# Kernel optimization log

Measured on AMD Instinct MI355X. Metric: run time of the kernel, lower is better.

Reference implementation:

```python
import jax, jax.numpy as jnp
import numpy as np

T, N, E, F_IN, C = 8, 50000, 800000, 64, 64


def setup_inputs() -> dict:
    key = jax.random.key(0)
    ks = jax.random.split(key, 32)
    inp = {
        "x": jax.random.normal(ks[0], (T, N, F_IN), dtype=jnp.float32),
        "edge_index": jax.random.randint(ks[1], (2, E), 0, N, dtype=jnp.int32),
        "edge_weight": jax.random.uniform(ks[2], (E,), dtype=jnp.float32),
    }
    s = 0.05
    names = ["xz", "hz", "xr", "hr", "xh", "hh"]
    for i, nm in enumerate(names):
        cin = F_IN if nm[0] == "x" else C
        inp[f"W{nm}0"] = jax.random.normal(ks[3 + 3 * i], (cin, C), dtype=jnp.float32) * s
        inp[f"W{nm}1"] = jax.random.normal(ks[4 + 3 * i], (cin, C), dtype=jnp.float32) * s
        inp[f"b{nm}"] = jax.random.normal(ks[5 + 3 * i], (C,), dtype=jnp.float32) * s
    inp["W_lin"] = jax.random.normal(ks[30], (C, 1), dtype=jnp.float32) * s
    inp["b_lin"] = jax.random.normal(ks[31], (1,), dtype=jnp.float32) * s
    return inp


def reference(x, edge_index, edge_weight,
              Wxz0, Wxz1, bxz, Whz0, Whz1, bhz,
              Wxr0, Wxr1, bxr, Whr0, Whr1, bhr,
              Wxh0, Wxh1, bxh, Whh0, Whh1, bhh,
              W_lin, b_lin):
    src, dst = edge_index[0], edge_index[1]
    n = x.shape[1]
    # sym-normalized L_hat = -D^{-1/2} A D^{-1/2} (ChebConv, lambda_max=2)
    deg = jnp.zeros((n,), x.dtype).at[src].add(edge_weight)
    dinv = jnp.where(deg > 0, jax.lax.rsqrt(jnp.maximum(deg, 1e-12)), 0.0)
    nw = -edge_weight * dinv[src] * dinv[dst]  # (E,)

    def cheb(v, W0, W1, b):
        # K=2 Chebyshev: v @ W0 + (L_hat v) @ W1 + b ; v: (T, N, Cin)
        msgs = nw[None, :, None] * v[:, src, :]          # (T, E, Cin)
        tx1 = jnp.zeros_like(v).at[:, dst, :].add(msgs)  # scatter-add over nodes
        return v @ W0 + tx1 @ W1 + b

    H = jnp.zeros(x.shape[:2] + (Whz0.shape[0],), x.dtype)  # H=None -> zeros
    Z = jax.nn.sigmoid(cheb(x, Wxz0, Wxz1, bxz) + cheb(H, Whz0, Whz1, bhz))
    R = jax.nn.sigmoid(cheb(x, Wxr0, Wxr1, bxr) + cheb(H, Whr0, Whr1, bhr))
    Ht = jnp.tanh(cheb(x, Wxh0, Wxh1, bxh) + cheb(R * H, Whh0, Whh1, bhh))
    H = Z * H + (1.0 - Z) * Ht
    h = jax.nn.relu(H)
    return h @ W_lin + b_lin
```

## Files before the change

kernel.cpp:

```cpp
#include <hip/hip_runtime.h>

#define T_ 8
#define N_ 50000
#define E_ 800000
#define C_ 64

typedef __attribute__((ext_vector_type(8))) short bf16x8;
typedef __attribute__((ext_vector_type(4))) float f32x4;

__device__ inline short f2bf(float f) {
    union { float f; unsigned int u; } v; v.f = f;
    unsigned int u = v.u + 0x7FFFu + ((v.u >> 16) & 1u);
    return (short)(u >> 16);
}
__device__ inline float bf2f_lo(unsigned int u) {
    union { unsigned int u; float f; } v; v.u = u << 16;
    return v.f;
}
__device__ inline float bf2f_hi(unsigned int u) {
    union { unsigned int u; float f; } v; v.u = u & 0xffff0000u;
    return v.f;
}

#define SCAN_TILES 49

__global__ __launch_bounds__(256) void fused_prep_kernel(
        const int* __restrict__ src, const int* __restrict__ dst,
        const float* __restrict__ w,
        float* __restrict__ degw, int* __restrict__ cnt,
        const float* __restrict__ x, unsigned short* __restrict__ xb,
        const float* __restrict__ Wz0, const float* __restrict__ Wz1,
        const float* __restrict__ Wh0, const float* __restrict__ Wh1,
        short* __restrict__ swz) {
    if (blockIdx.x < 3125) {
        int e = blockIdx.x * 256 + threadIdx.x;
        if (e < E_) {
            atomicAdd(&degw[src[e]], w[e]);
            atomicAdd(&cnt[dst[e]], 1);
        }
    } else if (blockIdx.x < 15625) {
        int id = (blockIdx.x - 3125) * 256 + threadIdx.x;
        int c8 = id & 7;
        int t = (id >> 3) & 7;
        int n = id >> 6;
        const float* xr = x + ((long long)t * N_ + n) * C_ + c8 * 8;
        float4 a = *(const float4*)(xr);
        float4 b = *(const float4*)(xr + 4);
        bf16x8 o;
        o[0] = f2bf(a.x); o[1] = f2bf(a.y); o[2] = f2bf(a.z); o[3] = f2bf(a.w);
        o[4] = f2bf(b.x); o[5] = f2bf(b.y); o[6] = f2bf(b.z); o[7] = f2bf(b.w);
        *(bf16x8*)(xb + (long long)id * 8) = o;
    } else {
        int idx = (blockIdx.x - 15625) * 256 + threadIdx.x;
        int j = idx & 7;
        int lane = (idx >> 3) & 63;
        int kb = (idx >> 9) & 1;
        int c = (idx >> 10) & 3;
        int mat = idx >> 12;
        const float* W = (mat == 0) ? Wz0 : (mat == 1) ? Wz1 : (mat == 2) ? Wh0 : Wh1;
        int k = kb * 32 + (lane >> 4) * 8 + j;
        int n = c * 16 + (lane & 15);
        swz[idx] = f2bf(W[k * 64 + n]);
    }
}

__global__ __launch_bounds__(1024) void scan_a_kernel(const int* __restrict__ cnt,
                                                      int* __restrict__ rowptr,
                                                      int* __restrict__ tsum) {
    __shared__ int wsum[16];
    int tid = threadIdx.x, lane = tid & 63, wid = tid >> 6;
    int idx = blockIdx.x * 1024 + tid;
    int orig = (idx < N_) ? cnt[idx] : 0;
    int v = orig;
#pragma unroll
    for (int off = 1; off < 64; off <<= 1) {
        int u = __shfl_up(v, off);
        if (lane >= off) v += u;
    }
    if (lane == 63) wsum[wid] = v;
    __syncthreads();
    if (wid == 0) {
        int s = (lane < 16) ? wsum[lane] : 0;
#pragma unroll
        for (int off = 1; off < 16; off <<= 1) {
            int u = __shfl_up(s, off);
            if (lane >= off) s += u;
        }
        if (lane < 16) wsum[lane] = s;
    }
    __syncthreads();
    int wpre = wid ? wsum[wid - 1] : 0;
    if (idx < N_) rowptr[idx] = wpre + v - orig;
    if (tid == 0) tsum[blockIdx.x] = wsum[15];
}

__global__ __launch_bounds__(1024) void scan_b_kernel(const int* __restrict__ tsum,
                                                      int* __restrict__ rowptr) {
    __shared__ int soff[SCAN_TILES];
    __shared__ int stot;
    int tid = threadIdx.x, lane = tid & 63, wid = tid >> 6;
    if (wid == 0) {
        int own = (lane < SCAN_TILES) ? tsum[lane] : 0;
        int s = own;
#pragma unroll
        for (int off = 1; off < 64; off <<= 1) {
            int u = __shfl_up(s, off);
            if (lane >= off) s += u;
        }
        if (lane < SCAN_TILES) soff[lane] = s - own;
        if (lane == SCAN_TILES - 1) stot = s;
    }
    __syncthreads();
    int off = soff[blockIdx.x];
    int idx = blockIdx.x * 1024 + tid;
    if (idx < N_) rowptr[idx] += off;
    if (blockIdx.x == SCAN_TILES - 1 && tid == 0) rowptr[N_] = stot;
}

__global__ void reorder_kernel(const int* __restrict__ src, const int* __restrict__ dst,
                               const float* __restrict__ w, const float* __restrict__ degw,
                               int* __restrict__ rowptr, int2* __restrict__ es, int E) {
    int e = blockIdx.x * blockDim.x + threadIdx.x;
    if (e < E) {
        int s = src[e], d = dst[e];
        float ds = degw[s], dd = degw[d];
        float is = ds > 0.f ? rsqrtf(fmaxf(ds, 1e-12f)) : 0.f;
        float id = dd > 0.f ? rsqrtf(fmaxf(dd, 1e-12f)) : 0.f;
        float nwv = -w[e] * is * id;
        int pos = atomicAdd(&rowptr[d], 1);
        es[pos] = make_int2(s, __float_as_int(nwv));
    }
}

#define ACC8(W, V)                                                       \
    acc[0] += (W) * bf2f_lo((V).x); acc[1] += (W) * bf2f_hi((V).x);      \
    acc[2] += (W) * bf2f_lo((V).y); acc[3] += (W) * bf2f_hi((V).y);      \
    acc[4] += (W) * bf2f_lo((V).z); acc[5] += (W) * bf2f_hi((V).z);      \
    acc[6] += (W) * bf2f_lo((V).w); acc[7] += (W) * bf2f_hi((V).w);

__global__ __launch_bounds__(256) void gather_node_kernel(
        const int* __restrict__ rowptr, const int2* __restrict__ es,
        const unsigned short* __restrict__ xb, const short* __restrict__ swz,
        const float* __restrict__ bxz, const float* __restrict__ bhz,
        const float* __restrict__ bxh, const float* __restrict__ bhh,
        const float* __restrict__ Wlin, const float* __restrict__ blin,
        float* __restrict__ out) {
    __shared__ unsigned short ltx[32 * 72];
    __shared__ float laz[2][16][65];

    int lane = threadIdx.x & 63;
    int wid = threadIdx.x >> 6;
    int base = blockIdx.x * 4;

    {
        int d = base + wid;
        int t = lane >> 3;
        int oct = lane & 7;
        int start = d ? rowptr[d - 1] : 0;
        int end = rowptr[d];
        float acc[8] = {0.f, 0.f, 0.f, 0.f, 0.f, 0.f, 0.f, 0.f};
        const unsigned short* xbase = xb + lane * 8;
        for (int b0 = start; b0 < end; b0 += 64) {
            int m = end - b0;
            if (m > 64) m = 64;
            int2 pk = (lane < m) ? es[b0 + lane] : make_int2(0, 0);
            int k = 0;
            for (; k + 3 < m; k += 4) {
                int s0 = __shfl(pk.x, k);
                int s1 = __shfl(pk.x, k + 1);
                int s2 = __shfl(pk.x, k + 2);
                int s3 = __shfl(pk.x, k + 3);
                uint4 v0 = *(const uint4*)(xbase + (long long)s0 * 512);
                uint4 v1 = *(const uint4*)(xbase + (long long)s1 * 512);
                uint4 v2 = *(const uint4*)(xbase + (long long)s2 * 512);
                uint4 v3 = *(const uint4*)(xbase + (long long)s3 * 512);
                float w0 = __int_as_float(__shfl(pk.y, k));
                float w1 = __int_as_float(__shfl(pk.y, k + 1));
                float w2 = __int_as_float(__shfl(pk.y, k + 2));
                float w3 = __int_as_float(__shfl(pk.y, k + 3));
                ACC8(w0, v0);
                ACC8(w1, v1);
                ACC8(w2, v2);
                ACC8(w3, v3);
            }
            for (; k < m; ++k) {
                int s0 = __shfl(pk.x, k);
                float w0 = __int_as_float(__shfl(pk.y, k));
                uint4 v0 = *(const uint4*)(xbase + (long long)s0 * 512);
                ACC8(w0, v0);
            }
        }
        uint4 o;
        o.x = (unsigned int)(unsigned short)f2bf(acc[0]) |
              ((unsigned int)(unsigned short)f2bf(acc[1]) << 16);
        o.y = (unsigned int)(unsigned short)f2bf(acc[2]) |
              ((unsigned int)(unsigned short)f2bf(acc[3]) << 16);
        o.z = (unsigned int)(unsigned short)f2bf(acc[4]) |
              ((unsigned int)(unsigned short)f2bf(acc[5]) << 16);
        o.w = (unsigned int)(unsigned short)f2bf(acc[6]) |
              ((unsigned int)(unsigned short)f2bf(acc[7]) << 16);
        int r = wid * 8 + t;
        *(uint4*)(ltx + r * 72 + oct * 8) = o;
    }
    __syncthreads();

    int mt = wid >> 1;
    int g = wid & 1;
    int c16 = lane & 15;
    int kq = lane >> 4;
    int r_blk = mt * 16 + c16;
    const unsigned short* xr = xb + (long long)(base * 8 + r_blk) * C_ + kq * 8;
    bf16x8 ax0 = *(const bf16x8*)(xr);
    bf16x8 ax1 = *(const bf16x8*)(xr + 32);
    bf16x8 at0 = *(const bf16x8*)(ltx + r_blk * 72 + kq * 8);
    bf16x8 at1 = *(const bf16x8*)(ltx + r_blk * 72 + 32 + kq * 8);

    const float* bA = g ? bxh : bxz;
    const float* bB = g ? bhh : bhz;
    const short* wA = swz + (2 * g) * 4096 + lane * 8;
    const short* wB = swz + (2 * g + 1) * 4096 + lane * 8;

    f32x4 a4[4];
#pragma unroll
    for (int c = 0; c < 4; ++c) {
        int col = c * 16 + c16;
        float bv = bA[col] + bB[col];
        a4[c] = (f32x4){bv, bv, bv, bv};
    }
#pragma unroll
    for (int c = 0; c < 4; ++c) {
        bf16x8 bA0 = *(const bf16x8*)(wA + (c * 2 + 0) * 512);
        bf16x8 bA1 = *(const bf16x8*)(wA + (c * 2 + 1) * 512);
        bf16x8 bB0 = *(const bf16x8*)(wB + (c * 2 + 0) * 512);
        bf16x8 bB1 = *(const bf16x8*)(wB + (c * 2 + 1) * 512);
        a4[c] = __builtin_amdgcn_mfma_f32_16x16x32_bf16(ax0, bA0, a4[c], 0, 0, 0);
        a4[c] = __builtin_amdgcn_mfma_f32_16x16x32_bf16(ax1, bA1, a4[c], 0, 0, 0);
        a4[c] = __builtin_amdgcn_mfma_f32_16x16x32_bf16(at0, bB0, a4[c], 0, 0, 0);
        a4[c] = __builtin_amdgcn_mfma_f32_16x16x32_bf16(at1, bB1, a4[c], 0, 0, 0);
    }

    if (g == 0) {
#pragma unroll
        for (int c = 0; c < 4; ++c)
#pragma unroll
            for (int r = 0; r < 4; ++r)
                laz[mt][kq * 4 + r][c * 16 + c16] = a4[c][r];
    }
    __syncthreads();
    if (g == 1) {
        float part[4] = {0.f, 0.f, 0.f, 0.f};
#pragma unroll
        for (int c = 0; c < 4; ++c) {
            int col = c * 16 + c16;
            float wl = Wlin[col];
#pragma unroll
            for (int r = 0; r < 4; ++r) {
                float a = laz[mt][kq * 4 + r][col];
                float b = a4[c][r];
                float z = 1.f / (1.f + __expf(-a));
                float aa = fabsf(b);
                float e = __expf(-2.f * aa);
                float ht = copysignf((1.f - e) / (1.f + e), b);
                float h = fmaxf((1.f - z) * ht, 0.f);
                part[r] += h * wl;
            }
        }
#pragma unroll
        for (int m = 1; m <= 8; m <<= 1) {
#pragma unroll
            for (int r = 0; r < 4; ++r) part[r] += __shfl_xor(part[r], m);
        }
        if (c16 == 0) {
            float bl = blin[0];
#pragma unroll
            for (int r = 0; r < 4; ++r) {
                int rb = mt * 16 + kq * 4 + r;
                out[(long long)(rb & 7) * N_ + base + (rb >> 3)] = part[r] + bl;
            }
        }
    }
}

extern "C" void kernel_launch(void* const* d_in, const int* in_sizes, int n_in,
                              void* d_out, int out_size, void* d_ws, size_t ws_size,
                              hipStream_t stream) {
    const float* x    = (const float*)d_in[0];
    const int*   ei   = (const int*)d_in[1];
    const float* w    = (const float*)d_in[2];
    const float* Wxz0 = (const float*)d_in[3];
    const float* Wxz1 = (const float*)d_in[4];
    const float* bxz  = (const float*)d_in[5];
    const float* bhz  = (const float*)d_in[8];
    const float* Wxh0 = (const float*)d_in[15];
    const float* Wxh1 = (const float*)d_in[16];
    const float* bxh  = (const float*)d_in[17];
    const float* bhh  = (const float*)d_in[20];
    const float* Wlin = (const float*)d_in[21];
    const float* blin = (const float*)d_in[22];
    float* out = (float*)d_out;

    const int* src = ei;
    const int* dst = ei + E_;

    char* ws = (char*)d_ws;
    size_t off = 0;
    auto alloc = [&](size_t bytes) {
        char* p = ws + off;
        off = (off + bytes + 511) & ~(size_t)511;
        return p;
    };
    short* swz             = (short*)alloc(4 * 4096 * sizeof(short));
    float* degw            = (float*)alloc((size_t)N_ * 4);
    int*   cnt             = (int*)alloc((size_t)N_ * 4);
    int*   rowptr          = (int*)alloc(((size_t)N_ + 1) * 4);
    int*   tsum            = (int*)alloc((size_t)SCAN_TILES * 4);
    int2*  es              = (int2*)alloc((size_t)E_ * 8);
    unsigned short* xb     = (unsigned short*)alloc((size_t)T_ * N_ * C_ * 2);

    hipMemsetAsync(degw, 0, (size_t)N_ * 4, stream);
    hipMemsetAsync(cnt, 0, (size_t)N_ * 4, stream);

    fused_prep_kernel<<<15689, 256, 0, stream>>>(src, dst, w, degw, cnt,
                                                 x, xb, Wxz0, Wxz1, Wxh0, Wxh1, swz);
    scan_a_kernel<<<SCAN_TILES, 1024, 0, stream>>>(cnt, rowptr, tsum);
    scan_b_kernel<<<SCAN_TILES, 1024, 0, stream>>>(tsum, rowptr);
    reorder_kernel<<<(E_ + 255) / 256, 256, 0, stream>>>(src, dst, w, degw, rowptr, es, E_);

    gather_node_kernel<<<N_ / 4, 256, 0, stream>>>(
        rowptr, es, xb, swz, bxz, bhz, bxh, bhh, Wlin, blin, out);
}
```

Before: 423.8 us.

## Replace CSR build with fixed-capacity per-node edge buckets and overflow list

Drops the two scan kernels and the reorder kernel by writing each edge directly into a per-destination bucket of fixed capacity during the degree-counting pass, with an overflow list for nodes beyond capacity. Edge normalization moves into the gather kernel, which computes rsqrt of source and destination degrees on the fly. The gather inner loop is unrolled to 8 outstanding loads. Risks: padded bucket storage costs memory and scattered writes, and the overflow path is a linear scan over all overflow entries for every high-degree node.

```diff
diff --git a/kernel.cpp b/kernel.cpp
--- a/kernel.cpp
+++ b/kernel.cpp
@@ -4,6 +4,7 @@
 #define N_ 50000
 #define E_ 800000
 #define C_ 64
+#define OVF_CAP 131072
 
 typedef __attribute__((ext_vector_type(8))) short bf16x8;
 typedef __attribute__((ext_vector_type(4))) float f32x4;
@@ -22,21 +23,27 @@
     return v.f;
 }
 
-#define SCAN_TILES 49
-
 __global__ __launch_bounds__(256) void fused_prep_kernel(
         const int* __restrict__ src, const int* __restrict__ dst,
         const float* __restrict__ w,
         float* __restrict__ degw, int* __restrict__ cnt,
+        int2* __restrict__ es, int cap,
+        int* __restrict__ ovfcnt, int4* __restrict__ ovf,
         const float* __restrict__ x, unsigned short* __restrict__ xb,
         const float* __restrict__ Wz0, const float* __restrict__ Wz1,
         const float* __restrict__ Wh0, const float* __restrict__ Wh1,
         short* __restrict__ swz) {
     if (blockIdx.x < 3125) {
         int e = blockIdx.x * 256 + threadIdx.x;
-        if (e < E_) {
-            atomicAdd(&degw[src[e]], w[e]);
-            atomicAdd(&cnt[dst[e]], 1);
+        int s = src[e], d = dst[e];
+        float wv = w[e];
+        atomicAdd(&degw[s], wv);
+        int pos = atomicAdd(&cnt[d], 1);
+        if (pos < cap) {
+            es[d * cap + pos] = make_int2(s, __float_as_int(wv));
+        } else {
+            int op = atomicAdd(ovfcnt, 1);
+            if (op < OVF_CAP) ovf[op] = make_int4(d, s, __float_as_int(wv), 0);
         }
     } else if (blockIdx.x < 15625) {
         int id = (blockIdx.x - 3125) * 256 + threadIdx.x;
@@ -64,74 +71,6 @@
     }
 }
 
-__global__ __launch_bounds__(1024) void scan_a_kernel(const int* __restrict__ cnt,
-                                                      int* __restrict__ rowptr,
-                                                      int* __restrict__ tsum) {
-    __shared__ int wsum[16];
-    int tid = threadIdx.x, lane = tid & 63, wid = tid >> 6;
-    int idx = blockIdx.x * 1024 + tid;
-    int orig = (idx < N_) ? cnt[idx] : 0;
-    int v = orig;
-#pragma unroll
-    for (int off = 1; off < 64; off <<= 1) {
-        int u = __shfl_up(v, off);
-        if (lane >= off) v += u;
-    }
-    if (lane == 63) wsum[wid] = v;
-    __syncthreads();
-    if (wid == 0) {
-        int s = (lane < 16) ? wsum[lane] : 0;
-#pragma unroll
-        for (int off = 1; off < 16; off <<= 1) {
-            int u = __shfl_up(s, off);
-            if (lane >= off) s += u;
-        }
-        if (lane < 16) wsum[lane] = s;
-    }
-    __syncthreads();
-    int wpre = wid ? wsum[wid - 1] : 0;
-    if (idx < N_) rowptr[idx] = wpre + v - orig;
-    if (tid == 0) tsum[blockIdx.x] = wsum[15];
-}
-
-__global__ __launch_bounds__(1024) void scan_b_kernel(const int* __restrict__ tsum,
-                                                      int* __restrict__ rowptr) {
-    __shared__ int soff[SCAN_TILES];
-    __shared__ int stot;
-    int tid = threadIdx.x, lane = tid & 63, wid = tid >> 6;
-    if (wid == 0) {
-        int own = (lane < SCAN_TILES) ? tsum[lane] : 0;
-        int s = own;
-#pragma unroll
-        for (int off = 1; off < 64; off <<= 1) {
-            int u = __shfl_up(s, off);
-            if (lane >= off) s += u;
-        }
-        if (lane < SCAN_TILES) soff[lane] = s - own;
-        if (lane == SCAN_TILES - 1) stot = s;
-    }
-    __syncthreads();
-    int off = soff[blockIdx.x];
-    int idx = blockIdx.x * 1024 + tid;
-    if (idx < N_) rowptr[idx] += off;
-    if (blockIdx.x == SCAN_TILES - 1 && tid == 0) rowptr[N_] = stot;
-}
-
-__global__ void reorder_kernel(const int* __restrict__ src, const int* __restrict__ dst,
-                               const float* __restrict__ w, const float* __restrict__ degw,
-                               int* __restrict__ rowptr, int2* __restrict__ es, int E) {
-    int e = blockIdx.x * blockDim.x + threadIdx.x;
-    if (e < E) {
-        int s = src[e], d = dst[e];
-        float ds = degw[s], dd = degw[d];
-        float is = ds > 0.f ? rsqrtf(fmaxf(ds, 1e-12f)) : 0.f;
-        float id = dd > 0.f ? rsqrtf(fmaxf(dd, 1e-12f)) : 0.f;
-        float nwv = -w[e] * is * id;
-        int pos = atomicAdd(&rowptr[d], 1);
-        es[pos] = make_int2(s, __float_as_int(nwv));
-    }
-}
-
 #define ACC8(W, V)                                                       \
     acc[0] += (W) * bf2f_lo((V).x); acc[1] += (W) * bf2f_hi((V).x);      \
     acc[2] += (W) * bf2f_lo((V).y); acc[3] += (W) * bf2f_hi((V).y);      \
@@ -139,7 +78,9 @@
     acc[6] += (W) * bf2f_lo((V).w); acc[7] += (W) * bf2f_hi((V).w);
 
 __global__ __launch_bounds__(256) void gather_node_kernel(
-        const int* __restrict__ rowptr, const int2* __restrict__ es,
+        const int* __restrict__ cnt, const int2* __restrict__ es, int cap,
+        const float* __restrict__ degw,
+        const int* __restrict__ ovfcnt, const int4* __restrict__ ovf,
         const unsigned short* __restrict__ xb, const short* __restrict__ swz,
         const float* __restrict__ bxz, const float* __restrict__ bhz,
         const float* __restrict__ bxh, const float* __restrict__ bhh,
@@ -156,51 +97,64 @@
         int d = base + wid;
         int t = lane >> 3;
         int oct = lane & 7;
-        int start = d ? rowptr[d - 1] : 0;
-        int end = rowptr[d];
+        int m = cnt[d];
+        int mb = m < cap ? m : cap;
+        float dd = degw[d];
+        float id = dd > 0.f ? rsqrtf(fmaxf(dd, 1e-12f)) : 0.f;
+
+        int2 pk = (lane < mb) ? es[d * cap + lane] : make_int2(0, 0);
+        float dsrc = degw[pk.x];
+        float is = dsrc > 0.f ? rsqrtf(fmaxf(dsrc, 1e-12f)) : 0.f;
+        float nw_l = -__int_as_float(pk.y) * is * id;
+
         float acc[8] = {0.f, 0.f, 0.f, 0.f, 0.f, 0.f, 0.f, 0.f};
         const unsigned short* xbase = xb + lane * 8;
-        for (int b0 = start; b0 < end; b0 += 64) {
-            int m = end - b0;
-            if (m > 64) m = 64;
-            int2 pk = (lane < m) ? es[b0 + lane] : make_int2(0, 0);
-            int k = 0;
-            for (; k + 3 < m; k += 4) {
-                int s0 = __shfl(pk.x, k);
-                int s1 = __shfl(pk.x, k + 1);
-                int s2 = __shfl(pk.x, k + 2);
-                int s3 = __shfl(pk.x, k + 3);
-                uint4 v0 = *(const uint4*)(xbase + (long long)s0 * 512);
-                uint4 v1 = *(const uint4*)(xbase + (long long)s1 * 512);
-                uint4 v2 = *(const uint4*)(xbase + (long long)s2 * 512);
-                uint4 v3 = *(const uint4*)(xbase + (long long)s3 * 512);
-                float w0 = __int_as_float(__shfl(pk.y, k));
-                float w1 = __int_as_float(__shfl(pk.y, k + 1));
-                float w2 = __int_as_float(__shfl(pk.y, k + 2));
-                float w3 = __int_as_float(__shfl(pk.y, k + 3));
-                ACC8(w0, v0);
-                ACC8(w1, v1);
-                ACC8(w2, v2);
-                ACC8(w3, v3);
-            }
-            for (; k < m; ++k) {
-                int s0 = __shfl(pk.x, k);
-                float w0 = __int_as_float(__shfl(pk.y, k));
-                uint4 v0 = *(const uint4*)(xbase + (long long)s0 * 512);
-                ACC8(w0, v0);
-            }
-        }
-        uint4 o;
-        o.x = (unsigned int)(unsigned short)f2bf(acc[0]) |
-              ((unsigned int)(unsigned short)f2bf(acc[1]) << 16);
-        o.y = (unsigned int)(unsigned short)f2bf(acc[2]) |
-              ((unsigned int)(unsigned short)f2bf(acc[3]) << 16);
-        o.z = (unsigned int)(unsigned short)f2bf(acc[4]) |
-              ((unsigned int)(unsigned short)f2bf(acc[5]) << 16);
-        o.w = (unsigned int)(unsigned short)f2bf(acc[6]) |
-              ((unsigned int)(unsigned short)f2bf(acc[7]) << 16);
+        int k = 0;
+        for (; k + 7 < mb; k += 8) {
+            int ss[8]; float ww[8];
+#pragma unroll
+            for (int j = 0; j < 8; ++j) {
+                ss[j] = __shfl(pk.x, k + j);
+                ww[j] = __shfl(nw_l, k + j);
+            }
+            uint4 vv[8];
+#pragma unroll
+            for (int j = 0; j < 8; ++j)
+                vv[j] = *(const uint4*)(xbase + (long long)ss[j] * 512);
+#pragma unroll
+            for (int j = 0; j < 8; ++j) { ACC8(ww[j], vv[j]); }
+        }
+        for (; k < mb; ++k) {
+            int s0 = __shfl(pk.x, k);
+            float w0 = __shfl(nw_l, k);
+            uint4 v0 = *(const uint4*)(xbase + (long long)s0 * 512);
+            ACC8(w0, v0);
+        }
+        if (m > cap) {
+            int oc = *ovfcnt;
+            if (oc > OVF_CAP) oc = OVF_CAP;
+            for (int i = 0; i < oc; ++i) {
+                int4 o = ovf[i];
+                if (o.x == d) {
+                    float ds = degw[o.y];
+                    float is2 = ds > 0.f ? rsqrtf(fmaxf(ds, 1e-12f)) : 0.f;
+                    float w0 = -__int_as_float(o.z) * is2 * id;
+                    uint4 v0 = *(const uint4*)(xbase + (long long)o.y * 512);
+                    ACC8(w0, v0);
+                }
+            }
+        }
+        uint4 ob;
+        ob.x = (unsigned int)(unsigned short)f2bf(acc[0]) |
+               ((unsigned int)(unsigned short)f2bf(acc[1]) << 16);
+        ob.y = (unsigned int)(unsigned short)f2bf(acc[2]) |
+               ((unsigned int)(unsigned short)f2bf(acc[3]) << 16);
+        ob.z = (unsigned int)(unsigned short)f2bf(acc[4]) |
+               ((unsigned int)(unsigned short)f2bf(acc[5]) << 16);
+        ob.w = (unsigned int)(unsigned short)f2bf(acc[6]) |
+               ((unsigned int)(unsigned short)f2bf(acc[7]) << 16);
         int r = wid * 8 + t;
-        *(uint4*)(ltx + r * 72 + oct * 8) = o;
+        *(uint4*)(ltx + r * 72 + oct * 8) = ob;
     }
     __syncthreads();
 
@@ -309,23 +263,29 @@
         off = (off + bytes + 511) & ~(size_t)511;
         return p;
     };
-    short* swz             = (short*)alloc(4 * 4096 * sizeof(short));
-    float* degw            = (float*)alloc((size_t)N_ * 4);
-    int*   cnt             = (int*)alloc((size_t)N_ * 4);
-    int*   rowptr          = (int*)alloc(((size_t)N_ + 1) * 4);
-    int*   tsum            = (int*)alloc((size_t)SCAN_TILES * 4);
-    int2*  es              = (int2*)alloc((size_t)E_ * 8);
-    unsigned short* xb     = (unsigned short*)alloc((size_t)T_ * N_ * C_ * 2);
+    short* swz         = (short*)alloc(4 * 4096 * sizeof(short));
+    float* degw        = (float*)alloc((size_t)N_ * 4);
+    int*   cnt         = (int*)alloc((size_t)N_ * 4);
+    int*   ovfcnt      = (int*)alloc(512);
+    int4*  ovf         = (int4*)alloc((size_t)OVF_CAP * 16);
+    unsigned short* xb = (unsigned short*)alloc((size_t)T_ * N_ * C_ * 2);
+    size_t fixed = off;
+
+    int cap = 16;
+    for (int c : {64, 48, 32, 24}) {
+        if (fixed + (size_t)N_ * c * 8 + 512 <= ws_size) { cap = c; break; }
+    }
+    int2* es = (int2*)alloc((size_t)N_ * cap * 8);
 
     hipMemsetAsync(degw, 0, (size_t)N_ * 4, stream);
     hipMemsetAsync(cnt, 0, (size_t)N_ * 4, stream);
+    hipMemsetAsync(ovfcnt, 0, 4, stream);
 
     fused_prep_kernel<<<15689, 256, 0, stream>>>(src, dst, w, degw, cnt,
+                                                 es, cap, ovfcnt, ovf,
                                                  x, xb, Wxz0, Wxz1, Wxh0, Wxh1, swz);
-    scan_a_kernel<<<SCAN_TILES, 1024, 0, stream>>>(cnt, rowptr, tsum);
-    scan_b_kernel<<<SCAN_TILES, 1024, 0, stream>>>(tsum, rowptr);
-    reorder_kernel<<<(E_ + 255) / 256, 256, 0, stream>>>(src, dst, w, degw, rowptr, es, E_);
 
     gather_node_kernel<<<N_ / 4, 256, 0, stream>>>(
-        rowptr, es, xb, swz, bxz, bhz, bxh, bhh, Wlin, blin, out);
-}
+        cnt, es, cap, degw, ovfcnt, ovf, xb, swz,
+        bxz, bhz, bxh, bhh, Wlin, blin, out);
+}
```

New measurement: 408.0 us. 1.04x faster.
